# Kernel optimization log

Measured on AMD Instinct MI355X. Metric: run time of the kernel, lower is better.

The kernel has to match this reference:

```python
import jax, jax.numpy as jnp
import numpy as np
import math

B, N, DEG, D = 128, 512, 8, 128
E = B * N * DEG
K1 = math.ceil(0.8 * N)    # 410 nodes kept per graph after pool1
K2 = math.ceil(0.8 * K1)   # 328 nodes kept per graph after pool2


def setup_inputs() -> dict:
    key = jax.random.key(0)
    ks = jax.random.split(key, 24)
    x = jax.random.normal(ks[0], (B * N, D), jnp.float32)
    # random edges within each graph, then offset to global node ids
    src_l = jax.random.randint(ks[1], (B, N * DEG), 0, N)
    dst_l = jax.random.randint(ks[2], (B, N * DEG), 0, N)
    offs = (jnp.arange(B) * N)[:, None]
    edge_index = jnp.stack([(src_l + offs).reshape(-1), (dst_l + offs).reshape(-1)]).astype(jnp.int32)
    w = lambda k, s: (jax.random.normal(k, s, jnp.float32) * 0.05)
    return {
        "x": x, "edge_index": edge_index,
        "W1r": w(ks[3], (D, 128)), "W1n": w(ks[4], (D, 128)), "b1": jnp.zeros((128,), jnp.float32),
        "p1": w(ks[5], (128,)),
        "W2r": w(ks[6], (128, 128)), "W2n": w(ks[7], (128, 128)), "b2": jnp.zeros((128,), jnp.float32),
        "p2": w(ks[8], (128,)),
        "lw1": w(ks[9], (256, 128)), "lb1": jnp.zeros((128,), jnp.float32),
        "lw2": w(ks[10], (128, 64)), "lb2": jnp.zeros((64,), jnp.float32),
        "lw3": w(ks[11], (64, 1)), "lb3": jnp.zeros((1,), jnp.float32),
    }


def _conv(h, src, dst, Wr, Wn, b):
    # GraphConv-style spatio-temporal message passing, sum aggregation
    msg = h[src] @ Wn                                   # [E, 128]
    agg = jax.ops.segment_sum(msg, dst, num_segments=B * N)
    return h @ Wr + agg + b


def _topk_mask(score, k, prev_mask):
    # per-graph top-k node selection (TopKPooling); restrict to prev_mask
    s = jnp.where(prev_mask, score, -jnp.inf).reshape(B, N)
    idx = jax.lax.top_k(s, k)[1]                        # [B, k]
    m = jnp.zeros((B, N), bool).at[jnp.arange(B)[:, None], idx].set(True)
    return m.reshape(B * N)


def _readout(h, mask, k):
    # concat of global max pool and global mean pool over kept nodes
    hm = jnp.where(mask[:, None], h, -jnp.inf).reshape(B, N, -1)
    gmax = hm.max(axis=1)
    gmean = (h * mask[:, None].astype(h.dtype)).reshape(B, N, -1).sum(axis=1) / k
    return jnp.concatenate([gmax, gmean], axis=1)       # [B, 256]


def reference(x, edge_index, W1r, W1n, b1, p1, W2r, W2n, b2, p2, lw1, lb1, lw2, lb2, lw3, lb3):
    src, dst = edge_index[0], edge_index[1]
    # conv1 + relu
    h = jax.nn.relu(_conv(x, src, dst, W1r, W1n, b1))
    # pool1: score = h.p/||p||, keep top-K1, gate by tanh(score)
    s1 = h @ p1 / jnp.linalg.norm(p1)
    m1 = _topk_mask(s1, K1, jnp.ones(B * N, bool))
    h = h * (jnp.tanh(s1) * m1.astype(h.dtype))[:, None]
    x1 = _readout(h, m1, K1)
    # conv2 + relu (dropped nodes have zero features -> zero messages)
    h = jax.nn.relu(_conv(h, src, dst, W2r, W2n, b2))
    s2 = h @ p2 / jnp.linalg.norm(p2)
    m2 = _topk_mask(s2, K2, m1)
    h = h * (jnp.tanh(s2) * m2.astype(h.dtype))[:, None]
    x2 = _readout(h, m2, K2)
    # MLP head (bn1/bn2 are defined but unused in the original forward; dropout is eval-mode identity)
    z = x1 + x2
    z = jax.nn.relu(z @ lw1 + lb1)
    z = jax.nn.relu(z @ lw2 + lb2)
    return jax.nn.sigmoid(z @ lw3 + lb3).squeeze(-1)    # [B]
```

## Files before the change

### kernel.cpp

```cpp
#include <hip/hip_runtime.h>
#include <math.h>

constexpr int B = 128;
constexpr int N = 512;
constexpr int DEG = 8;
constexpr int D = 128;
constexpr int E = B * N * DEG;
constexpr int EPG = N * DEG;
constexpr int NN = B * N;
constexpr int K1 = 410;
constexpr int K2 = 328;
constexpr int PADDEG = 16;
constexpr int CAP = 32;

typedef __attribute__((ext_vector_type(8))) short short8;
typedef __attribute__((ext_vector_type(4))) float f32x4;

__device__ __forceinline__ unsigned short f2bf(float f) {
    unsigned int u = __float_as_uint(f);
    unsigned int r = (u + 0x7fffu + ((u >> 16) & 1u)) >> 16;
    return (unsigned short)r;
}
__device__ __forceinline__ float bf2f(unsigned short h) {
    return __uint_as_float(((unsigned int)h) << 16);
}

__global__ __launch_bounds__(256) void k_prepw(const float* __restrict__ W0,
                                               const float* __restrict__ W1,
                                               const float* __restrict__ W2,
                                               const float* __restrict__ W3,
                                               unsigned short* __restrict__ wt,
                                               int* __restrict__ ccnt) {
    const float* Ws[4] = {W0, W1, W2, W3};
    const int m = blockIdx.x >> 6;
    const int idx = (blockIdx.x & 63) * 256 + threadIdx.x;
    ccnt[blockIdx.x * 256 + threadIdx.x] = 0;
    const float* src = Ws[m];
    unsigned short* dH = wt + (size_t)m * 32768;
    unsigned short* dL = dH + 16384;
    int kk = idx >> 7, n = idx & 127;
    float v = src[idx];
    unsigned short h = f2bf(v);
    unsigned short l = f2bf(v - bf2f(h));
    dH[n * 128 + kk] = h;
    dL[n * 128 + kk] = l;
}

__global__ __launch_bounds__(256) void k_count(const int* __restrict__ ei,
                                               int* __restrict__ ccnt,
                                               int* __restrict__ csrcp) {
    const int e = blockIdx.x * 256 + threadIdx.x;
    const int s = ei[e];
    const int d = ei[E + e];
    const int pos = atomicAdd(&ccnt[d], 1);
    if (pos < CAP) csrcp[(size_t)d * CAP + pos] = s;
}

__global__ __launch_bounds__(256) void k_sortpad(int* __restrict__ ccnt,
                                                 int* __restrict__ csrcp) {
    const int n = blockIdx.x * 256 + threadIdx.x;
    const int deg = min(ccnt[n], CAP);
    int a[CAP];
    #pragma unroll
    for (int j = 0; j < CAP / 4; ++j)
        *(int4*)&a[4 * j] = *(const int4*)&csrcp[(size_t)n * CAP + 4 * j];
    #pragma unroll
    for (int k = 0; k < CAP; ++k)
        if (k >= deg) a[k] = 0x7fffffff;
    #pragma unroll
    for (int k = 2; k <= CAP; k <<= 1) {
        #pragma unroll
        for (int j = k >> 1; j > 0; j >>= 1) {
            #pragma unroll
            for (int i = 0; i < CAP; ++i) {
                const int l = i ^ j;
                if (l > i) {
                    const bool dir = ((i & k) == 0);
                    int x = a[i], y = a[l];
                    if ((x > y) == dir) { a[i] = y; a[l] = x; }
                }
            }
        }
    }
    #pragma unroll
    for (int j = 0; j < CAP / 4; ++j)
        *(int4*)&csrcp[(size_t)n * CAP + 4 * j] =
            make_int4(a[4 * j], a[4 * j + 1], a[4 * j + 2], a[4 * j + 3]);
}

__global__ __launch_bounds__(256, 2) void k_gather(const float* __restrict__ feat,
                                                   const float* __restrict__ gate,
                                                   const int* __restrict__ ccnt,
                                                   const int* __restrict__ csrcp,
                                                   float* __restrict__ aggout) {
    const int bid = blockIdx.x;
    const int xcd = bid & 7;
    const int j = bid >> 3;
    const int g = ((j & 15) << 3) | xcd;
    const int chunk = j >> 4;
    const int t = threadIdx.x;
    const int lane = t & 31, grp = t >> 5;
    const int fo = lane * 4;
    #pragma unroll
    for (int it = 0; it < 4; ++it) {
        const int n = g * N + chunk * 32 + it * 8 + grp;
        const int deg = min(ccnt[n], CAP);
        int idx[PADDEG];
        *(int4*)&idx[0]  = *(const int4*)&csrcp[(size_t)n * CAP + 0];
        *(int4*)&idx[4]  = *(const int4*)&csrcp[(size_t)n * CAP + 4];
        *(int4*)&idx[8]  = *(const int4*)&csrcp[(size_t)n * CAP + 8];
        *(int4*)&idx[12] = *(const int4*)&csrcp[(size_t)n * CAP + 12];
        float4 acc = make_float4(0.f, 0.f, 0.f, 0.f);
        #pragma unroll
        for (int k = 0; k < PADDEG; ++k) {
            if (k < deg) {
                float wk = gate ? gate[idx[k]] : 1.0f;
                float4 v = *(const float4*)&feat[(size_t)idx[k] * D + fo];
                acc.x = fmaf(v.x, wk, acc.x);
                acc.y = fmaf(v.y, wk, acc.y);
                acc.z = fmaf(v.z, wk, acc.z);
                acc.w = fmaf(v.w, wk, acc.w);
            }
        }
        if (deg > PADDEG) {
            for (int k = PADDEG; k < deg; ++k) {
                int ix = csrcp[(size_t)n * CAP + k];
                float gt = gate ? gate[ix] : 1.0f;
                float4 v = *(const float4*)&feat[(size_t)ix * D + fo];
                acc.x = fmaf(v.x, gt, acc.x);
                acc.y = fmaf(v.y, gt, acc.y);
                acc.z = fmaf(v.z, gt, acc.z);
                acc.w = fmaf(v.w, gt, acc.w);
            }
        }
        *(float4*)&aggout[(size_t)n * D + fo] = acc;
    }
}

__global__ __launch_bounds__(256, 2) void k_gemm(const float* __restrict__ A0,
                                                 const float* __restrict__ gateA,
                                                 const float* __restrict__ A1,
                                                 const unsigned short* __restrict__ W0t,
                                                 const unsigned short* __restrict__ W1t,
                                                 const float* __restrict__ bias,
                                                 const float* __restrict__ pvec,
                                                 float* __restrict__ out,
                                                 float* __restrict__ sun) {
    __shared__ unsigned short AsH[128 * 40], AsL[128 * 40];
    __shared__ unsigned short BsH[128 * 40], BsL[128 * 40];
    __shared__ float red[128 * 33];
    const int t = threadIdx.x;
    const int r0 = blockIdx.x * 128;
    const int w = t >> 6, lane = t & 63;
    const int lr = lane & 15, kg = (lane >> 4) * 8;
    const int wm = (w >> 1) * 64, wn = (w & 1) * 64;
    const int arow = t >> 1, kb = (t & 1) * 16;
    const float ga = gateA ? gateA[r0 + arow] : 1.0f;

    f32x4 acc[4][4];
    #pragma unroll
    for (int mt = 0; mt < 4; ++mt)
        #pragma unroll
        for (int nt = 0; nt < 4; ++nt)
            acc[mt][nt] = (f32x4)(0.f);

    for (int phase = 0; phase < 2; ++phase) {
        const float* Ap = phase ? A1 : A0;
        const unsigned short* WH = phase ? W1t : W0t;
        const unsigned short* WL = WH + 16384;
        const float gmul = phase ? 1.0f : ga;
        for (int c = 0; c < 4; ++c) {
            const int k0 = c * 32;
            __syncthreads();
            #pragma unroll
            for (int i = 0; i < 4; ++i) {
                float4 av = *(const float4*)&Ap[(size_t)(r0 + arow) * D + k0 + kb + i * 4];
                av.x *= gmul; av.y *= gmul; av.z *= gmul; av.w *= gmul;
                unsigned int h0 = f2bf(av.x), h1 = f2bf(av.y), h2 = f2bf(av.z), h3 = f2bf(av.w);
                uint2 ph; ph.x = h0 | (h1 << 16); ph.y = h2 | (h3 << 16);
                *(uint2*)&AsH[arow * 40 + kb + i * 4] = ph;
                unsigned int l0 = f2bf(av.x - bf2f(h0)), l1 = f2bf(av.y - bf2f(h1));
                unsigned int l2 = f2bf(av.z - bf2f(h2)), l3 = f2bf(av.w - bf2f(h3));
                uint2 pl; pl.x = l0 | (l1 << 16); pl.y = l2 | (l3 << 16);
                *(uint2*)&AsL[arow * 40 + kb + i * 4] = pl;
            }
            {
                const int part = t & 3;
                #pragma unroll
                for (int rep = 0; rep < 2; ++rep) {
                    const int n = (t >> 2) + rep * 64;
                    *(int4*)&BsH[n * 40 + part * 8] = *(const int4*)&WH[n * 128 + k0 + part * 8];
                    *(int4*)&BsL[n * 40 + part * 8] = *(const int4*)&WL[n * 128 + k0 + part * 8];
                }
            }
            __syncthreads();
            short8 aH[4], aL[4], bH[4], bL[4];
            #pragma unroll
            for (int mt = 0; mt < 4; ++mt) {
                aH[mt] = *(const short8*)&AsH[(wm + mt * 16 + lr) * 40 + kg];
                aL[mt] = *(const short8*)&AsL[(wm + mt * 16 + lr) * 40 + kg];
            }
            #pragma unroll
            for (int nt = 0; nt < 4; ++nt) {
                bH[nt] = *(const short8*)&BsH[(wn + nt * 16 + lr) * 40 + kg];
                bL[nt] = *(const short8*)&BsL[(wn + nt * 16 + lr) * 40 + kg];
            }
            #pragma unroll
            for (int mt = 0; mt < 4; ++mt)
                #pragma unroll
                for (int nt = 0; nt < 4; ++nt) {
                    acc[mt][nt] = __builtin_amdgcn_mfma_f32_16x16x32_bf16(aH[mt], bH[nt], acc[mt][nt], 0, 0, 0);
                    acc[mt][nt] = __builtin_amdgcn_mfma_f32_16x16x32_bf16(aH[mt], bL[nt], acc[mt][nt], 0, 0, 0);
                    acc[mt][nt] = __builtin_amdgcn_mfma_f32_16x16x32_bf16(aL[mt], bH[nt], acc[mt][nt], 0, 0, 0);
                }
        }
    }
    float bb[4], pv[4];
    #pragma unroll
    for (int nt = 0; nt < 4; ++nt) {
        bb[nt] = bias[wn + nt * 16 + lr];
        pv[nt] = pvec[wn + nt * 16 + lr];
    }
    #pragma unroll
    for (int mt = 0; mt < 4; ++mt) {
        #pragma unroll
        for (int r = 0; r < 4; ++r) {
            const int rowl = wm + mt * 16 + (lane >> 4) * 4 + r;
            const int row = r0 + rowl;
            float part = 0.f;
            #pragma unroll
            for (int nt = 0; nt < 4; ++nt) {
                float v = acc[mt][nt][r] + bb[nt];
                v = fmaxf(v, 0.f);
                out[(size_t)row * D + wn + nt * 16 + lr] = v;
                part = fmaf(v, pv[nt], part);
            }
            red[rowl * 33 + (w & 1) * 16 + lr] = part;
        }
    }
    __syncthreads();
    if (t < 128) {
        float s = 0.f;
        #pragma unroll
        for (int j = 0; j < 32; ++j) s += red[t * 33 + j];
        sun[r0 + t] = s;
    }
}

__global__ __launch_bounds__(1024) void k_topk_readout(const float* __restrict__ sun,
                                                       const float* __restrict__ p,
                                                       const float* __restrict__ prevmask,
                                                       int K, float invK,
                                                       const float* __restrict__ h,
                                                       float* __restrict__ gate,
                                                       float* __restrict__ mask,
                                                       float* __restrict__ xout) {
    __shared__ float ls[512];
    __shared__ float lg[512];
    __shared__ float lm[512];
    __shared__ float red[128];
    __shared__ float smax[16][64];
    __shared__ float ssum[16][64];
    __shared__ float norm_s;
    const int bid = blockIdx.x;
    const int g = bid >> 1, half = bid & 1;
    const int t = threadIdx.x;
    if (t < 512) {
        const int n = g * N + t;
        float s = sun[n];
        if (prevmask && prevmask[n] == 0.0f) s = -INFINITY;
        ls[t] = s;
    }
    if (t < 128) { float pvv = p[t]; red[t] = pvv * pvv; }
    __syncthreads();
    if (t < 64) red[t] += red[t + 64];
    __syncthreads();
    if (t < 32) red[t] += red[t + 32];
    __syncthreads();
    if (t == 0) {
        float s = 0.f;
        #pragma unroll
        for (int i = 0; i < 32; ++i) s += red[i];
        norm_s = sqrtf(s);
    }
    __syncthreads();
    if (t < 512) {
        const float s = ls[t];
        int cnt = 0;
        for (int jj = 0; jj < 512; ++jj) {
            float sj = ls[jj];
            cnt += (sj > s || (sj == s && jj < t)) ? 1 : 0;
        }
        const bool keep = cnt < K;
        const float gv = keep ? tanhf(s / norm_s) : 0.0f;
        const float mv = keep ? 1.0f : 0.0f;
        lg[t] = gv; lm[t] = mv;
        gate[g * N + t] = gv; mask[g * N + t] = mv;
    }
    __syncthreads();
    const int f = half * 64 + (t & 63), sub = t >> 6;
    float vmax = -INFINITY, vsum = 0.f;
    for (int nl = sub; nl < N; nl += 16) {
        const float v = h[(size_t)(g * N + nl) * D + f] * lg[nl];
        vsum += v;
        if (lm[nl] != 0.f) vmax = fmaxf(vmax, v);
    }
    smax[sub][t & 63] = vmax;
    ssum[sub][t & 63] = vsum;
    __syncthreads();
    if (t < 64) {
        float m = smax[0][t], s = ssum[0][t];
        #pragma unroll
        for (int k = 1; k < 16; ++k) { m = fmaxf(m, smax[k][t]); s += ssum[k][t]; }
        xout[g * 256 + half * 64 + t] = m;
        xout[g * 256 + 128 + half * 64 + t] = s * invK;
    }
}

__global__ __launch_bounds__(128) void k_mlp(const float* __restrict__ X1,
                                             const float* __restrict__ X2,
                                             const float* __restrict__ lw1,
                                             const float* __restrict__ lb1,
                                             const float* __restrict__ lw2,
                                             const float* __restrict__ lb2,
                                             const float* __restrict__ lw3,
                                             const float* __restrict__ lb3,
                                             float* __restrict__ out) {
    __shared__ float z[256];
    __shared__ float o1[128];
    __shared__ float o2p[64];
    const int g = blockIdx.x, t = threadIdx.x;
    z[t] = X1[g * 256 + t] + X2[g * 256 + t];
    z[t + 128] = X1[g * 256 + 128 + t] + X2[g * 256 + 128 + t];
    __syncthreads();
    float a = lb1[t];
    for (int i = 0; i < 256; ++i) a = fmaf(z[i], lw1[i * 128 + t], a);
    o1[t] = fmaxf(a, 0.f);
    __syncthreads();
    if (t < 64) {
        float b = lb2[t];
        for (int i = 0; i < 128; ++i) b = fmaf(o1[i], lw2[i * 64 + t], b);
        o2p[t] = fmaxf(b, 0.f) * lw3[t];
    }
    __syncthreads();
    if (t == 0) {
        float sacc = lb3[0];
        for (int i = 0; i < 64; ++i) sacc += o2p[i];
        out[g] = 1.f / (1.f + expf(-sacc));
    }
}

extern "C" void kernel_launch(void* const* d_in, const int* in_sizes, int n_in,
                              void* d_out, int out_size, void* d_ws, size_t ws_size,
                              hipStream_t stream) {
    const float* x    = (const float*)d_in[0];
    const int*   ei   = (const int*)d_in[1];
    const float* W1r  = (const float*)d_in[2];
    const float* W1n  = (const float*)d_in[3];
    const float* b1   = (const float*)d_in[4];
    const float* p1   = (const float*)d_in[5];
    const float* W2r  = (const float*)d_in[6];
    const float* W2n  = (const float*)d_in[7];
    const float* b2   = (const float*)d_in[8];
    const float* p2   = (const float*)d_in[9];
    const float* lw1  = (const float*)d_in[10];
    const float* lb1  = (const float*)d_in[11];
    const float* lw2  = (const float*)d_in[12];
    const float* lb2  = (const float*)d_in[13];
    const float* lw3  = (const float*)d_in[14];
    const float* lb3  = (const float*)d_in[15];
    float* out = (float*)d_out;

    char* w = (char*)d_ws;
    float* h1  = (float*)w; w += (size_t)NN * D * 4;
    float* h2  = (float*)w; w += (size_t)NN * D * 4;
    float* agg = (float*)w; w += (size_t)NN * D * 4;
    int* ccnt  = (int*)w;   w += (size_t)NN * 4;
    int* csrcp = (int*)w;   w += (size_t)NN * CAP * 4;
    unsigned short* wt = (unsigned short*)w; w += (size_t)4 * 2 * 16384 * 2;
    float* sun = (float*)w; w += (size_t)NN * 4;
    float* g1  = (float*)w; w += (size_t)NN * 4;
    float* m1  = (float*)w; w += (size_t)NN * 4;
    float* g2  = (float*)w; w += (size_t)NN * 4;
    float* m2  = (float*)w; w += (size_t)NN * 4;
    float* X1  = (float*)w; w += (size_t)B * 256 * 4;
    float* X2  = (float*)w; w += (size_t)B * 256 * 4;

    const unsigned short* wt1r = wt;
    const unsigned short* wt1n = wt + 1 * 32768;
    const unsigned short* wt2r = wt + 2 * 32768;
    const unsigned short* wt2n = wt + 3 * 32768;

    k_prepw<<<256, 256, 0, stream>>>(W1r, W1n, W2r, W2n, wt, ccnt);
    k_count<<<E / 256, 256, 0, stream>>>(ei, ccnt, csrcp);
    k_sortpad<<<NN / 256, 256, 0, stream>>>(ccnt, csrcp);

    k_gather<<<2048, 256, 0, stream>>>(x, nullptr, ccnt, csrcp, agg);
    k_gemm<<<NN / 128, 256, 0, stream>>>(x, nullptr, agg, wt1r, wt1n, b1, p1, h1, sun);
    k_topk_readout<<<2 * B, 1024, 0, stream>>>(sun, p1, nullptr, K1, 1.0f / (float)K1, h1, g1, m1, X1);

    k_gather<<<2048, 256, 0, stream>>>(h1, g1, ccnt, csrcp, agg);
    k_gemm<<<NN / 128, 256, 0, stream>>>(h1, g1, agg, wt2r, wt2n, b2, p2, h2, sun);
    k_topk_readout<<<2 * B, 1024, 0, stream>>>(sun, p2, m1, K2, 1.0f / (float)K2, h2, g2, m2, X2);

    k_mlp<<<B, 128, 0, stream>>>(X1, X2, lw1, lb1, lw2, lb2, lw3, lb3, out);
}
```

Measured before the change: 285.9 us.

## Use 512-thread GEMM blocks with smaller per-wave tiles and aliased reduction smem

The fused conv GEMM now runs 8 waves per 128-row block instead of 4. Each wave computes a 32x64 tile, which halves the accumulator registers per wave. The reduction buffer now aliases the A-tile shared memory behind an extra barrier, cutting LDS use so more blocks can be resident. Tile staging is rewritten so each thread loads 8 elements of A and one int4 of each B half. The cost is that every wave now rereads the B fragments, adding LDS traffic per MFMA.

```diff
diff --git a/kernel.cpp b/kernel.cpp
--- a/kernel.cpp
+++ b/kernel.cpp
@@ -137,7 +137,7 @@
     }
 }
 
-__global__ __launch_bounds__(256, 2) void k_gemm(const float* __restrict__ A0,
+__global__ __launch_bounds__(512, 2) void k_gemm(const float* __restrict__ A0,
                                                  const float* __restrict__ gateA,
                                                  const float* __restrict__ A1,
                                                  const unsigned short* __restrict__ W0t,
@@ -146,20 +146,22 @@
                                                  const float* __restrict__ pvec,
                                                  float* __restrict__ out,
                                                  float* __restrict__ sun) {
-    __shared__ unsigned short AsH[128 * 40], AsL[128 * 40];
+    __shared__ unsigned short AsBuf[2 * 128 * 40];
     __shared__ unsigned short BsH[128 * 40], BsL[128 * 40];
-    __shared__ float red[128 * 33];
+    unsigned short* AsH = AsBuf;
+    unsigned short* AsL = AsBuf + 128 * 40;
+    float* red = (float*)AsBuf;
     const int t = threadIdx.x;
     const int r0 = blockIdx.x * 128;
     const int w = t >> 6, lane = t & 63;
     const int lr = lane & 15, kg = (lane >> 4) * 8;
-    const int wm = (w >> 1) * 64, wn = (w & 1) * 64;
-    const int arow = t >> 1, kb = (t & 1) * 16;
+    const int wm = (w >> 1) * 32, wn = (w & 1) * 64;
+    const int arow = t >> 2, kpart = (t & 3) * 8;
     const float ga = gateA ? gateA[r0 + arow] : 1.0f;
 
-    f32x4 acc[4][4];
-    #pragma unroll
-    for (int mt = 0; mt < 4; ++mt)
+    f32x4 acc[2][4];
+    #pragma unroll
+    for (int mt = 0; mt < 2; ++mt)
         #pragma unroll
         for (int nt = 0; nt < 4; ++nt)
             acc[mt][nt] = (f32x4)(0.f);
@@ -172,31 +174,29 @@
         for (int c = 0; c < 4; ++c) {
             const int k0 = c * 32;
             __syncthreads();
+            {
+                float4 a0 = *(const float4*)&Ap[(size_t)(r0 + arow) * D + k0 + kpart];
+                float4 a1 = *(const float4*)&Ap[(size_t)(r0 + arow) * D + k0 + kpart + 4];
+                float vals[8] = {a0.x * gmul, a0.y * gmul, a0.z * gmul, a0.w * gmul,
+                                 a1.x * gmul, a1.y * gmul, a1.z * gmul, a1.w * gmul};
+                unsigned int ph[4], pl[4];
+                #pragma unroll
+                for (int jj = 0; jj < 4; ++jj) {
+                    unsigned int h0 = f2bf(vals[2 * jj]), h1 = f2bf(vals[2 * jj + 1]);
+                    ph[jj] = h0 | (h1 << 16);
+                    unsigned int l0 = f2bf(vals[2 * jj] - bf2f((unsigned short)h0));
+                    unsigned int l1 = f2bf(vals[2 * jj + 1] - bf2f((unsigned short)h1));
+                    pl[jj] = l0 | (l1 << 16);
+                }
+                *(int4*)&AsH[arow * 40 + kpart] = make_int4(ph[0], ph[1], ph[2], ph[3]);
+                *(int4*)&AsL[arow * 40 + kpart] = make_int4(pl[0], pl[1], pl[2], pl[3]);
+            }
+            *(int4*)&BsH[arow * 40 + kpart] = *(const int4*)&WH[arow * 128 + k0 + kpart];
+            *(int4*)&BsL[arow * 40 + kpart] = *(const int4*)&WL[arow * 128 + k0 + kpart];
+            __syncthreads();
+            short8 aH[2], aL[2], bH[4], bL[4];
             #pragma unroll
-            for (int i = 0; i < 4; ++i) {
-                float4 av = *(const float4*)&Ap[(size_t)(r0 + arow) * D + k0 + kb + i * 4];
-                av.x *= gmul; av.y *= gmul; av.z *= gmul; av.w *= gmul;
-                unsigned int h0 = f2bf(av.x), h1 = f2bf(av.y), h2 = f2bf(av.z), h3 = f2bf(av.w);
-                uint2 ph; ph.x = h0 | (h1 << 16); ph.y = h2 | (h3 << 16);
-                *(uint2*)&AsH[arow * 40 + kb + i * 4] = ph;
-                unsigned int l0 = f2bf(av.x - bf2f(h0)), l1 = f2bf(av.y - bf2f(h1));
-                unsigned int l2 = f2bf(av.z - bf2f(h2)), l3 = f2bf(av.w - bf2f(h3));
-                uint2 pl; pl.x = l0 | (l1 << 16); pl.y = l2 | (l3 << 16);
-                *(uint2*)&AsL[arow * 40 + kb + i * 4] = pl;
-            }
-            {
-                const int part = t & 3;
-                #pragma unroll
-                for (int rep = 0; rep < 2; ++rep) {
-                    const int n = (t >> 2) + rep * 64;
-                    *(int4*)&BsH[n * 40 + part * 8] = *(const int4*)&WH[n * 128 + k0 + part * 8];
-                    *(int4*)&BsL[n * 40 + part * 8] = *(const int4*)&WL[n * 128 + k0 + part * 8];
-                }
-            }
-            __syncthreads();
-            short8 aH[4], aL[4], bH[4], bL[4];
-            #pragma unroll
-            for (int mt = 0; mt < 4; ++mt) {
+            for (int mt = 0; mt < 2; ++mt) {
                 aH[mt] = *(const short8*)&AsH[(wm + mt * 16 + lr) * 40 + kg];
                 aL[mt] = *(const short8*)&AsL[(wm + mt * 16 + lr) * 40 + kg];
             }
@@ -206,7 +206,7 @@
                 bL[nt] = *(const short8*)&BsL[(wn + nt * 16 + lr) * 40 + kg];
             }
             #pragma unroll
-            for (int mt = 0; mt < 4; ++mt)
+            for (int mt = 0; mt < 2; ++mt)
                 #pragma unroll
                 for (int nt = 0; nt < 4; ++nt) {
                     acc[mt][nt] = __builtin_amdgcn_mfma_f32_16x16x32_bf16(aH[mt], bH[nt], acc[mt][nt], 0, 0, 0);
@@ -215,6 +215,7 @@
                 }
         }
     }
+    __syncthreads();
     float bb[4], pv[4];
     #pragma unroll
     for (int nt = 0; nt < 4; ++nt) {
@@ -222,7 +223,7 @@
         pv[nt] = pvec[wn + nt * 16 + lr];
     }
     #pragma unroll
-    for (int mt = 0; mt < 4; ++mt) {
+    for (int mt = 0; mt < 2; ++mt) {
         #pragma unroll
         for (int r = 0; r < 4; ++r) {
             const int rowl = wm + mt * 16 + (lane >> 4) * 4 + r;
@@ -396,11 +397,11 @@
     k_sortpad<<<NN / 256, 256, 0, stream>>>(ccnt, csrcp);
 
     k_gather<<<2048, 256, 0, stream>>>(x, nullptr, ccnt, csrcp, agg);
-    k_gemm<<<NN / 128, 256, 0, stream>>>(x, nullptr, agg, wt1r, wt1n, b1, p1, h1, sun);
+    k_gemm<<<NN / 128, 512, 0, stream>>>(x, nullptr, agg, wt1r, wt1n, b1, p1, h1, sun);
     k_topk_readout<<<2 * B, 1024, 0, stream>>>(sun, p1, nullptr, K1, 1.0f / (float)K1, h1, g1, m1, X1);
 
     k_gather<<<2048, 256, 0, stream>>>(h1, g1, ccnt, csrcp, agg);
-    k_gemm<<<NN / 128, 256, 0, stream>>>(h1, g1, agg, wt2r, wt2n, b2, p2, h2, sun);
+    k_gemm<<<NN / 128, 512, 0, stream>>>(h1, g1, agg, wt2r, wt2n, b2, p2, h2, sun);
     k_topk_readout<<<2 * B, 1024, 0, stream>>>(sun, p2, m1, K2, 1.0f / (float)K2, h2, g2, m2, X2);
 
     k_mlp<<<B, 128, 0, stream>>>(X1, X2, lw1, lb1, lw2, lb2, lw3, lb3, out);
```

Result: no change. 284.1 us (-0.6%).
